# Optimization experiments

Hardware: AMD Instinct MI355X
Metric: run time of the kernel (lower is better)

Reference implementation:

```python
import jax, jax.numpy as jnp
import numpy as np

B, SIDES, L = 8192, 2, 64   # batch, (left,right) trees, leaves per tree (complete binary tree)
V, D, C, R = 10000, 128, 128, 7  # vocab, word_dim, cpr_dim, num_rels


def setup_inputs() -> dict:
    key = jax.random.key(0)
    ks = jax.random.split(key, 9)
    s = 0.05
    return {
        "tokens": jax.random.randint(ks[0], (B, SIDES, L), 0, V, dtype=jnp.int32),
        "voc_w": jax.random.normal(ks[1], (V, D), dtype=jnp.float32) * s,
        "voc_b": jax.random.normal(ks[2], (D,), dtype=jnp.float32) * s,
        "cps_w": jax.random.normal(ks[3], (D, 2 * D), dtype=jnp.float32) * s,
        "cps_b": jax.random.normal(ks[4], (D,), dtype=jnp.float32) * s,
        "cpr_w": jax.random.normal(ks[5], (C, 2 * D), dtype=jnp.float32) * s,
        "cpr_b": jax.random.normal(ks[6], (C,), dtype=jnp.float32) * s,
        "sm_w": jax.random.normal(ks[7], (R, C), dtype=jnp.float32) * s,
        "sm_b": jax.random.normal(ks[8], (R,), dtype=jnp.float32) * s,
    }


def reference(tokens, voc_w, voc_b, cps_w, cps_b, cpr_w, cpr_b, sm_w, sm_b):
    # Leaf composition: one-hot @ Linear(voc_size, word_dim) == embedding gather + bias
    h = voc_w[tokens] + voc_b  # [B, 2, L, D]
    # Level-by-level composition of complete binary trees: cat(left,right) -> cps -> tanh
    n = h.shape[2]
    while n > 1:
        h = h.reshape(h.shape[0], SIDES, n // 2, 2 * h.shape[-1])  # adjacent pairs -> concat
        h = jnp.tanh(jnp.einsum('bsnk,dk->bsnd', h, cps_w) + cps_b)
        n //= 2
    root = h.reshape(h.shape[0], -1)  # [B, 2*D]: cat(left_cps, right_cps)
    z = jax.nn.leaky_relu(root @ cpr_w.T + cpr_b)  # LeakyReLU default slope 0.01
    return jax.nn.softmax(z @ sm_w.T + sm_b, axis=-1)  # [B, R]
```

## Files before the change

kernel.cpp:

```cpp
#include <hip/hip_runtime.h>
#include <hip/hip_bf16.h>


typedef __attribute__((ext_vector_type(8))) short bf16x8;
typedef __attribute__((ext_vector_type(4))) float f32x4;

#define VOCN (10000 * 128)
#define CPSN (128 * 256)
#define CPRN (128 * 256)

__device__ __forceinline__ uint pk2(float a, float b) {
  union { __hip_bfloat162 h2; uint u; } cv;
  cv.h2 = __float22bfloat162_rn(make_float2(a, b));
  return cv.u;
}
__device__ __forceinline__ float2 up2(uint u) {
  union { uint u; __hip_bfloat162 h2; } cv; cv.u = u;
  return __bfloat1622float2(cv.h2);
}
__device__ __forceinline__ float fast_tanh(float x) {
  float e = __builtin_amdgcn_exp2f(x * 2.88539008f);
  return 1.0f - 2.0f * __builtin_amdgcn_rcpf(e + 1.0f);
}

__global__ void prep_kernel(const float* __restrict__ voc_w, const float* __restrict__ voc_b,
                            const float* __restrict__ cps_w, const float* __restrict__ cpr_w,
                            ushort* __restrict__ ws) {
  const int i4 = (blockIdx.x * 256 + threadIdx.x) * 4;
  if (i4 >= VOCN + CPSN + CPRN) return;
  float4 v;
  if (i4 < VOCN) {
    v = *(const float4*)(voc_w + i4);
    const float4 bb = *(const float4*)(voc_b + (i4 & 127));
    v.x += bb.x; v.y += bb.y; v.z += bb.z; v.w += bb.w;
  } else if (i4 < VOCN + CPSN) {
    v = *(const float4*)(cps_w + (i4 - VOCN));
  } else {
    v = *(const float4*)(cpr_w + (i4 - VOCN - CPSN));
  }
  uint2 w; w.x = pk2(v.x, v.y); w.y = pk2(v.z, v.w);
  *(uint2*)(ws + i4) = w;
}

#define MFMA16(Ax, Bx, Cx) __builtin_amdgcn_mfma_f32_16x16x32_bf16(Ax, Bx, Cx, 0, 0, 0)

template<int TOFF>
__device__ __forceinline__ void tile16(const char* hb, const bf16x8 (&A)[2][8],
                                       int RL, int RR, f32x4& aA, f32x4& aB) {
  bf16x8 bl[4], br[4];
#pragma unroll
  for (int q = 0; q < 4; ++q) {
    bl[q] = *(const bf16x8*)(hb + RL + TOFF + q * 4096);
    br[q] = *(const bf16x8*)(hb + RR + TOFF + q * 4096);
  }
#pragma unroll
  for (int q = 0; q < 4; ++q) {
    aA = MFMA16(A[0][q], bl[q], aA);
    aB = MFMA16(A[1][q], bl[q], aB);
  }
#pragma unroll
  for (int q = 0; q < 4; ++q) {
    aA = MFMA16(A[0][4 + q], br[q], aA);
    aB = MFMA16(A[1][4 + q], br[q], aB);
  }
}

template<int TOFF>
__device__ __forceinline__ void wtile(char* hb, int W, const f32x4& aA, const f32x4& aB) {
  uint2 w0, w1;
  w0.x = pk2(fast_tanh(aA[0]), fast_tanh(aA[1]));
  w0.y = pk2(fast_tanh(aA[2]), fast_tanh(aA[3]));
  w1.x = pk2(fast_tanh(aB[0]), fast_tanh(aB[1]));
  w1.y = pk2(fast_tanh(aB[2]), fast_tanh(aB[3]));
  *(uint2*)(hb + W + TOFF) = w0;
  *(uint2*)(hb + W + TOFF + 2048) = w1;
}

template<int PRE>
__global__ __launch_bounds__(256, 4)
void trnn_kernel(const int* __restrict__ tokens,
                 const float* __restrict__ voc_w, const float* __restrict__ voc_b,
                 const float* __restrict__ cps_w, const float* __restrict__ cps_b,
                 const float* __restrict__ cpr_w, const float* __restrict__ cpr_b,
                 const float* __restrict__ sm_w, const float* __restrict__ sm_b,
                 const ushort* __restrict__ wsb, float* __restrict__ out) {
  __shared__ ushort h[16384];
  const int tid = threadIdx.x;
  const int lane = tid & 63, wv = tid >> 6;
  const int l15 = lane & 15, lh = lane >> 4;
  const int b = blockIdx.x;
  char* hb = (char*)h;

  const ushort* voc_bf = wsb;
  const ushort* cps_bf = wsb + VOCN;
  const ushort* cpr_bf = wsb + VOCN + CPSN;

  const int lhb = lh * 1024;
  const int lb16 = l15 * 16;
  const int RLa = lhb + lb16;
  const int RLb = lhb + 256 + lb16;
  const int RRa = lhb + 512 + lb16;
  const int RRb = lhb + 768 + lb16;
  const int t3 = ((l15 >> 3) & 1) << 14;
  const int RL3 = t3 + lhb + (l15 & 7) * 16;
  const int RR3 = RL3 + 128;
  const int t4 = ((l15 >> 2) & 1) << 14;
  const int RL4 = t4 + lhb + (l15 & 3) * 16;
  const int RR4 = RL4 + 64;
  const int t5 = ((l15 >> 1) & 1) << 14;
  const int RL5 = t5 + lhb + (l15 & 1) * 16;
  const int RR5 = RL5 + 32;
  const int t6 = (l15 & 1) << 14;
  const int RL6 = t6 + lhb;
  const int RR6 = RL6 + 16;
  const int dpart = (((wv * 32 + lh * 4) >> 3) << 10) + ((lh & 1) << 3);
  const int Wa = ((l15 & 1) * 16 + (l15 >> 1)) * 16 + dpart;
  const int Wb = Wa + 128;
  const int W2 = ((l15 & 1) * 8 + (l15 >> 1)) * 16 + dpart;
  const int W3 = t3 + (((l15 & 1) * 4 + ((l15 & 7) >> 1)) * 16) + dpart;
  const int W4 = t4 + (((l15 & 1) * 2 + ((l15 & 3) >> 1)) * 16) + dpart;
  const int W5 = t5 + ((l15 & 1) * 16) + dpart;
  const int W6 = t6 + dpart;

  bf16x8 A[2][8];
  f32x4 bias[2];
#pragma unroll
  for (int mt = 0; mt < 2; ++mt) {
    const int d = wv * 32 + mt * 16 + l15;
#pragma unroll
    for (int kt = 0; kt < 8; ++kt) {
      const int k = kt * 32 + lh * 8;
      if constexpr (PRE) {
        A[mt][kt] = *(const bf16x8*)(cps_bf + d * 256 + k);
      } else {
        const float* p = cps_w + d * 256 + k;
        float4 lo = *(const float4*)p, hi = *(const float4*)(p + 4);
        union { bf16x8 v; uint4 u; } f;
        f.u.x = pk2(lo.x, lo.y); f.u.y = pk2(lo.z, lo.w);
        f.u.z = pk2(hi.x, hi.y); f.u.w = pk2(hi.z, hi.w);
        A[mt][kt] = f.v;
      }
    }
    const float4 bb = *(const float4*)(cps_b + wv * 32 + mt * 16 + lh * 4);
    bias[mt][0] = bb.x; bias[mt][1] = bb.y; bias[mt][2] = bb.z; bias[mt][3] = bb.w;
  }

  {
    const int tree = tid >> 7, lf = (tid >> 1) & 63, half = tid & 1;
    const int tok = tokens[b * 128 + tree * 64 + lf];
    const int p = (lf & 1) * 32 + (lf >> 1);
    char* tp = hb + tree * 16384 + half * 8192 + p * 16;
    if constexpr (PRE) {
      const ushort* vr = voc_bf + tok * 128 + half * 64;
#pragma unroll
      for (int j = 0; j < 8; ++j) {
        const int c = (j + p) & 7;
        *(uint4*)(tp + c * 1024) = *(const uint4*)(vr + c * 8);
      }
    } else {
      const float* vw = voc_w + tok * 128 + half * 64;
      const float* vb = voc_b + half * 64;
#pragma unroll
      for (int j = 0; j < 8; ++j) {
        const int c = (j + p) & 7;
        float4 v0 = *(const float4*)(vw + c * 8);
        float4 v1 = *(const float4*)(vw + c * 8 + 4);
        float4 q0 = *(const float4*)(vb + c * 8);
        float4 q1 = *(const float4*)(vb + c * 8 + 4);
        uint4 w;
        w.x = pk2(v0.x + q0.x, v0.y + q0.y);
        w.y = pk2(v0.z + q0.z, v0.w + q0.w);
        w.z = pk2(v1.x + q1.x, v1.y + q1.y);
        w.w = pk2(v1.z + q1.z, v1.w + q1.w);
        *(uint4*)(tp + c * 1024) = w;
      }
    }
  }
  __syncthreads();

  {
    f32x4 a0 = bias[0], b0 = bias[1], a1 = bias[0], b1 = bias[1];
    f32x4 a2 = bias[0], b2 = bias[1], a3 = bias[0], b3 = bias[1];
    tile16<0>(hb, A, RLa, RRa, a0, b0);
    tile16<0>(hb, A, RLb, RRb, a1, b1);
    tile16<16384>(hb, A, RLa, RRa, a2, b2);
    tile16<16384>(hb, A, RLb, RRb, a3, b3);
    __syncthreads();
    wtile<0>(hb, Wa, a0, b0);
    wtile<0>(hb, Wb, a1, b1);
    wtile<16384>(hb, Wa, a2, b2);
    wtile<16384>(hb, Wb, a3, b3);
    __syncthreads();
  }
  {
    f32x4 a0 = bias[0], b0 = bias[1], a1 = bias[0], b1 = bias[1];
    tile16<0>(hb, A, RLa, RLb, a0, b0);
    tile16<16384>(hb, A, RLa, RLb, a1, b1);
    __syncthreads();
    wtile<0>(hb, W2, a0, b0);
    wtile<16384>(hb, W2, a1, b1);
    __syncthreads();
  }
  {
    f32x4 a0 = bias[0], b0 = bias[1];
    tile16<0>(hb, A, RL3, RR3, a0, b0);
    __syncthreads();
    wtile<0>(hb, W3, a0, b0);
    __syncthreads();
  }
  {
    f32x4 a0 = bias[0], b0 = bias[1];
    tile16<0>(hb, A, RL4, RR4, a0, b0);
    __syncthreads();
    if (l15 < 8) wtile<0>(hb, W4, a0, b0);
    __syncthreads();
  }
  {
    f32x4 a0 = bias[0], b0 = bias[1];
    tile16<0>(hb, A, RL5, RR5, a0, b0);
    __syncthreads();
    if (l15 < 4) wtile<0>(hb, W5, a0, b0);
    __syncthreads();
  }
  {
    f32x4 a0 = bias[0], b0 = bias[1];
    tile16<0>(hb, A, RL6, RR6, a0, b0);
    __syncthreads();
    if (l15 < 2) wtile<0>(hb, W6, a0, b0);
    __syncthreads();
  }


  {
    const int half = tid >> 7, c = tid & 127;
    const char* rp = hb + half * 16384;
    float acc = 0.f;
#pragma unroll 4
    for (int ch = 0; ch < 16; ++ch) {
      uint4 u = *(const uint4*)(rp + ch * 1024);
      float2 e0 = up2(u.x), e1 = up2(u.y), e2 = up2(u.z), e3 = up2(u.w);
      if constexpr (PRE) {
        uint4 wq = *(const uint4*)(cpr_bf + c * 256 + half * 128 + ch * 8);
        float2 w0 = up2(wq.x), w1 = up2(wq.y), w2 = up2(wq.z), w3 = up2(wq.w);
        acc += e0.x * w0.x + e0.y * w0.y + e1.x * w1.x + e1.y * w1.y
             + e2.x * w2.x + e2.y * w2.y + e3.x * w3.x + e3.y * w3.y;
      } else {
        const float* wr = cpr_w + c * 256 + half * 128 + ch * 8;
        float4 w0 = *(const float4*)wr, w1 = *(const float4*)(wr + 4);
        acc += e0.x * w0.x + e0.y * w0.y + e1.x * w0.z + e1.y * w0.w
             + e2.x * w1.x + e2.y * w1.y + e3.x * w1.z + e3.y * w1.w;
      }
    }
    *(float*)(hb + ((tid >> 4) << 10) + 512 + ((tid & 15) << 2)) = acc;
  }
  __syncthreads();
  if (tid < 128) {
    const float p0 = *(const float*)(hb + ((tid >> 4) << 10) + 512 + ((tid & 15) << 2));
    const int j1 = tid + 128;
    const float p1 = *(const float*)(hb + ((j1 >> 4) << 10) + 512 + ((j1 & 15) << 2));
    float z = p0 + p1 + cpr_b[tid];
    z = z > 0.f ? z : 0.01f * z;
    *(float*)(hb + 16384 + ((tid >> 3) << 10) + 768 + ((tid & 7) << 2)) = z;
  }
  __syncthreads();

  if (wv == 0) {
    const int i0 = lane, i1 = 64 + lane;
    const float za = *(const float*)(hb + 16384 + ((i0 >> 3) << 10) + 768 + ((i0 & 7) << 2));
    const float zc = *(const float*)(hb + 16384 + ((i1 >> 3) << 10) + 768 + ((i1 & 7) << 2));
    float p[7];
#pragma unroll
    for (int j = 0; j < 7; ++j)
      p[j] = za * sm_w[j * 128 + lane] + zc * sm_w[j * 128 + 64 + lane];
#pragma unroll
    for (int j = 0; j < 7; ++j) {
      float v = p[j];
#pragma unroll
      for (int off = 32; off >= 1; off >>= 1) v += __shfl_xor(v, off, 64);
      p[j] = v + sm_b[j];
    }
    float mx = p[0];
#pragma unroll
    for (int j = 1; j < 7; ++j) mx = fmaxf(mx, p[j]);
    float e[7], s = 0.f;
#pragma unroll
    for (int j = 0; j < 7; ++j) { e[j] = __expf(p[j] - mx); s += e[j]; }
    const float inv = 1.f / s;
    if (lane == 0) {
#pragma unroll
      for (int j = 0; j < 7; ++j) out[b * 7 + j] = e[j] * inv;
    }
  }
}

extern "C" void kernel_launch(void* const* d_in, const int* in_sizes, int n_in,
                              void* d_out, int out_size, void* d_ws, size_t ws_size,
                              hipStream_t stream) {
  const int*   tokens = (const int*)  d_in[0];
  const float* voc_w  = (const float*)d_in[1];
  const float* voc_b  = (const float*)d_in[2];
  const float* cps_w  = (const float*)d_in[3];
  const float* cps_b  = (const float*)d_in[4];
  const float* cpr_w  = (const float*)d_in[5];
  const float* cpr_b  = (const float*)d_in[6];
  const float* sm_w   = (const float*)d_in[7];
  const float* sm_b   = (const float*)d_in[8];
  float* out = (float*)d_out;

  const int B = in_sizes[0] / 128;
  const size_t need = (size_t)(VOCN + CPSN + CPRN) * sizeof(ushort);

  if (ws_size >= need) {
    ushort* ws = (ushort*)d_ws;
    const int tot4 = (VOCN + CPSN + CPRN) / 4;
    prep_kernel<<<(tot4 + 255) / 256, 256, 0, stream>>>(voc_w, voc_b, cps_w, cpr_w, ws);
    trnn_kernel<1><<<B, 256, 0, stream>>>(tokens, voc_w, voc_b, cps_w, cps_b,
                                          cpr_w, cpr_b, sm_w, sm_b, ws, out);
  } else {
    trnn_kernel<0><<<B, 256, 0, stream>>>(tokens, voc_w, voc_b, cps_w, cps_b,
                                          cpr_w, cpr_b, sm_w, sm_b,
                                          (const ushort*)d_ws, out);
  }
}
```

Baseline: 162.3 us.

## Process two batch elements per block and prefetch next embeddings during the tail

Each block now handles two consecutive batch samples, so the per-block load of the composition weights into registers is paid once for two trees. The leaf embeddings for the second sample are fetched into registers before the projection and softmax stage of the first sample, then written to shared memory afterwards to hide gather latency. The leaky-ReLU outputs move to a separate small shared array so the next leaves can be stored safely. The costs are half as many blocks, extra registers for the prefetch buffer, and an unrotated store order for the second sample's leaves that may add shared-memory bank conflicts.

```diff
diff --git a/kernel.cpp b/kernel.cpp
--- a/kernel.cpp
+++ b/kernel.cpp
@@ -85,10 +85,11 @@
                  const float* __restrict__ sm_w, const float* __restrict__ sm_b,
                  const ushort* __restrict__ wsb, float* __restrict__ out) {
   __shared__ ushort h[16384];
+  __shared__ float z2[128];
   const int tid = threadIdx.x;
   const int lane = tid & 63, wv = tid >> 6;
   const int l15 = lane & 15, lh = lane >> 4;
-  const int b = blockIdx.x;
+  const int b0 = blockIdx.x * 2;
   char* hb = (char*)h;
 
   const ushort* voc_bf = wsb;
@@ -145,24 +146,24 @@
     bias[mt][0] = bb.x; bias[mt][1] = bb.y; bias[mt][2] = bb.z; bias[mt][3] = bb.w;
   }
 
+  const int tree_e = tid >> 7, lf_e = (tid >> 1) & 63, half_e = tid & 1;
+  const int p_e = (lf_e & 1) * 32 + (lf_e >> 1);
+  char* tp = hb + tree_e * 16384 + half_e * 8192 + p_e * 16;
   {
-    const int tree = tid >> 7, lf = (tid >> 1) & 63, half = tid & 1;
-    const int tok = tokens[b * 128 + tree * 64 + lf];
-    const int p = (lf & 1) * 32 + (lf >> 1);
-    char* tp = hb + tree * 16384 + half * 8192 + p * 16;
+    const int tok = tokens[b0 * 128 + tree_e * 64 + lf_e];
     if constexpr (PRE) {
-      const ushort* vr = voc_bf + tok * 128 + half * 64;
+      const ushort* vr = voc_bf + tok * 128 + half_e * 64;
 #pragma unroll
       for (int j = 0; j < 8; ++j) {
-        const int c = (j + p) & 7;
+        const int c = (j + p_e) & 7;
         *(uint4*)(tp + c * 1024) = *(const uint4*)(vr + c * 8);
       }
     } else {
-      const float* vw = voc_w + tok * 128 + half * 64;
-      const float* vb = voc_b + half * 64;
+      const float* vw = voc_w + tok * 128 + half_e * 64;
+      const float* vb = voc_b + half_e * 64;
 #pragma unroll
       for (int j = 0; j < 8; ++j) {
-        const int c = (j + p) & 7;
+        const int c = (j + p_e) & 7;
         float4 v0 = *(const float4*)(vw + c * 8);
         float4 v1 = *(const float4*)(vw + c * 8 + 4);
         float4 q0 = *(const float4*)(vb + c * 8);
@@ -178,117 +179,150 @@
   }
   __syncthreads();
 
-  {
-    f32x4 a0 = bias[0], b0 = bias[1], a1 = bias[0], b1 = bias[1];
-    f32x4 a2 = bias[0], b2 = bias[1], a3 = bias[0], b3 = bias[1];
-    tile16<0>(hb, A, RLa, RRa, a0, b0);
-    tile16<0>(hb, A, RLb, RRb, a1, b1);
-    tile16<16384>(hb, A, RLa, RRa, a2, b2);
-    tile16<16384>(hb, A, RLb, RRb, a3, b3);
+  for (int r = 0; r < 2; ++r) {
+    {
+      f32x4 a0 = bias[0], b0v = bias[1], a1 = bias[0], b1 = bias[1];
+      f32x4 a2 = bias[0], b2 = bias[1], a3 = bias[0], b3 = bias[1];
+      tile16<0>(hb, A, RLa, RRa, a0, b0v);
+      tile16<0>(hb, A, RLb, RRb, a1, b1);
+      tile16<16384>(hb, A, RLa, RRa, a2, b2);
+      tile16<16384>(hb, A, RLb, RRb, a3, b3);
+      __syncthreads();
+      wtile<0>(hb, Wa, a0, b0v);
+      wtile<0>(hb, Wb, a1, b1);
+      wtile<16384>(hb, Wa, a2, b2);
+      wtile<16384>(hb, Wb, a3, b3);
+      __syncthreads();
+    }
+    {
+      f32x4 a0 = bias[0], b0v = bias[1], a1 = bias[0], b1 = bias[1];
+      tile16<0>(hb, A, RLa, RLb, a0, b0v);
+      tile16<16384>(hb, A, RLa, RLb, a1, b1);
+      __syncthreads();
+      wtile<0>(hb, W2, a0, b0v);
+      wtile<16384>(hb, W2, a1, b1);
+      __syncthreads();
+    }
+    {
+      f32x4 a0 = bias[0], b0v = bias[1];
+      tile16<0>(hb, A, RL3, RR3, a0, b0v);
+      __syncthreads();
+      wtile<0>(hb, W3, a0, b0v);
+      __syncthreads();
+    }
+    {
+      f32x4 a0 = bias[0], b0v = bias[1];
+      tile16<0>(hb, A, RL4, RR4, a0, b0v);
+      __syncthreads();
+      if (l15 < 8) wtile<0>(hb, W4, a0, b0v);
+      __syncthreads();
+    }
+    {
+      f32x4 a0 = bias[0], b0v = bias[1];
+      tile16<0>(hb, A, RL5, RR5, a0, b0v);
+      __syncthreads();
+      if (l15 < 4) wtile<0>(hb, W5, a0, b0v);
+      __syncthreads();
+    }
+    {
+      f32x4 a0 = bias[0], b0v = bias[1];
+      tile16<0>(hb, A, RL6, RR6, a0, b0v);
+      __syncthreads();
+      if (l15 < 2) wtile<0>(hb, W6, a0, b0v);
+      __syncthreads();
+    }
+
+    uint4 pf[8];
+    if (PRE && r == 0) {
+      const int tok1 = tokens[(b0 + 1) * 128 + tree_e * 64 + lf_e];
+      const ushort* vr = voc_bf + tok1 * 128 + half_e * 64;
+#pragma unroll
+      for (int j = 0; j < 8; ++j) pf[j] = *(const uint4*)(vr + j * 8);
+    }
+
+    {
+      const int half = tid >> 7, c = tid & 127;
+      const char* rp = hb + half * 16384;
+      float acc = 0.f;
+#pragma unroll 4
+      for (int ch = 0; ch < 16; ++ch) {
+        uint4 u = *(const uint4*)(rp + ch * 1024);
+        float2 e0 = up2(u.x), e1 = up2(u.y), e2 = up2(u.z), e3 = up2(u.w);
+        if constexpr (PRE) {
+          uint4 wq = *(const uint4*)(cpr_bf + c * 256 + half * 128 + ch * 8);
+          float2 w0 = up2(wq.x), w1 = up2(wq.y), w2 = up2(wq.z), w3 = up2(wq.w);
+          acc += e0.x * w0.x + e0.y * w0.y + e1.x * w1.x + e1.y * w1.y
+               + e2.x * w2.x + e2.y * w2.y + e3.x * w3.x + e3.y * w3.y;
+        } else {
+          const float* wr = cpr_w + c * 256 + half * 128 + ch * 8;
+          float4 w0 = *(const float4*)wr, w1 = *(const float4*)(wr + 4);
+          acc += e0.x * w0.x + e0.y * w0.y + e1.x * w0.z + e1.y * w0.w
+               + e2.x * w1.x + e2.y * w1.y + e3.x * w1.z + e3.y * w1.w;
+        }
+      }
+      *(float*)(hb + ((tid >> 4) << 10) + 512 + ((tid & 15) << 2)) = acc;
+    }
     __syncthreads();
-    wtile<0>(hb, Wa, a0, b0);
-    wtile<0>(hb, Wb, a1, b1);
-    wtile<16384>(hb, Wa, a2, b2);
-    wtile<16384>(hb, Wb, a3, b3);
+    if (tid < 128) {
+      const float p0 = *(const float*)(hb + ((tid >> 4) << 10) + 512 + ((tid & 15) << 2));
+      const int j1 = tid + 128;
+      const float p1 = *(const float*)(hb + ((j1 >> 4) << 10) + 512 + ((j1 & 15) << 2));
+      float z = p0 + p1 + cpr_b[tid];
+      z2[tid] = z > 0.f ? z : 0.01f * z;
+    }
     __syncthreads();
-  }
-  {
-    f32x4 a0 = bias[0], b0 = bias[1], a1 = bias[0], b1 = bias[1];
-    tile16<0>(hb, A, RLa, RLb, a0, b0);
-    tile16<16384>(hb, A, RLa, RLb, a1, b1);
-    __syncthreads();
-    wtile<0>(hb, W2, a0, b0);
-    wtile<16384>(hb, W2, a1, b1);
-    __syncthreads();
-  }
-  {
-    f32x4 a0 = bias[0], b0 = bias[1];
-    tile16<0>(hb, A, RL3, RR3, a0, b0);
-    __syncthreads();
-    wtile<0>(hb, W3, a0, b0);
-    __syncthreads();
-  }
-  {
-    f32x4 a0 = bias[0], b0 = bias[1];
-    tile16<0>(hb, A, RL4, RR4, a0, b0);
-    __syncthreads();
-    if (l15 < 8) wtile<0>(hb, W4, a0, b0);
-    __syncthreads();
-  }
-  {
-    f32x4 a0 = bias[0], b0 = bias[1];
-    tile16<0>(hb, A, RL5, RR5, a0, b0);
-    __syncthreads();
-    if (l15 < 4) wtile<0>(hb, W5, a0, b0);
-    __syncthreads();
-  }
-  {
-    f32x4 a0 = bias[0], b0 = bias[1];
-    tile16<0>(hb, A, RL6, RR6, a0, b0);
-    __syncthreads();
-    if (l15 < 2) wtile<0>(hb, W6, a0, b0);
-    __syncthreads();
-  }
-
-
-  {
-    const int half = tid >> 7, c = tid & 127;
-    const char* rp = hb + half * 16384;
-    float acc = 0.f;
-#pragma unroll 4
-    for (int ch = 0; ch < 16; ++ch) {
-      uint4 u = *(const uint4*)(rp + ch * 1024);
-      float2 e0 = up2(u.x), e1 = up2(u.y), e2 = up2(u.z), e3 = up2(u.w);
+
+    if (wv == 0) {
+      const float za = z2[lane];
+      const float zc = z2[64 + lane];
+      float p[7];
+#pragma unroll
+      for (int j = 0; j < 7; ++j)
+        p[j] = za * sm_w[j * 128 + lane] + zc * sm_w[j * 128 + 64 + lane];
+#pragma unroll
+      for (int j = 0; j < 7; ++j) {
+        float v = p[j];
+#pragma unroll
+        for (int off = 32; off >= 1; off >>= 1) v += __shfl_xor(v, off, 64);
+        p[j] = v + sm_b[j];
+      }
+      float mx = p[0];
+#pragma unroll
+      for (int j = 1; j < 7; ++j) mx = fmaxf(mx, p[j]);
+      float e[7], s = 0.f;
+#pragma unroll
+      for (int j = 0; j < 7; ++j) { e[j] = __expf(p[j] - mx); s += e[j]; }
+      const float inv = 1.f / s;
+      if (lane == 0) {
+#pragma unroll
+        for (int j = 0; j < 7; ++j) out[(b0 + r) * 7 + j] = e[j] * inv;
+      }
+    }
+
+    if (r == 0) {
       if constexpr (PRE) {
-        uint4 wq = *(const uint4*)(cpr_bf + c * 256 + half * 128 + ch * 8);
-        float2 w0 = up2(wq.x), w1 = up2(wq.y), w2 = up2(wq.z), w3 = up2(wq.w);
-        acc += e0.x * w0.x + e0.y * w0.y + e1.x * w1.x + e1.y * w1.y
-             + e2.x * w2.x + e2.y * w2.y + e3.x * w3.x + e3.y * w3.y;
+#pragma unroll
+        for (int j = 0; j < 8; ++j)
+          *(uint4*)(tp + j * 1024) = pf[j];
       } else {
-        const float* wr = cpr_w + c * 256 + half * 128 + ch * 8;
-        float4 w0 = *(const float4*)wr, w1 = *(const float4*)(wr + 4);
-        acc += e0.x * w0.x + e0.y * w0.y + e1.x * w0.z + e1.y * w0.w
-             + e2.x * w1.x + e2.y * w1.y + e3.x * w1.z + e3.y * w1.w;
-      }
-    }
-    *(float*)(hb + ((tid >> 4) << 10) + 512 + ((tid & 15) << 2)) = acc;
-  }
-  __syncthreads();
-  if (tid < 128) {
-    const float p0 = *(const float*)(hb + ((tid >> 4) << 10) + 512 + ((tid & 15) << 2));
-    const int j1 = tid + 128;
-    const float p1 = *(const float*)(hb + ((j1 >> 4) << 10) + 512 + ((j1 & 15) << 2));
-    float z = p0 + p1 + cpr_b[tid];
-    z = z > 0.f ? z : 0.01f * z;
-    *(float*)(hb + 16384 + ((tid >> 3) << 10) + 768 + ((tid & 7) << 2)) = z;
-  }
-  __syncthreads();
-
-  if (wv == 0) {
-    const int i0 = lane, i1 = 64 + lane;
-    const float za = *(const float*)(hb + 16384 + ((i0 >> 3) << 10) + 768 + ((i0 & 7) << 2));
-    const float zc = *(const float*)(hb + 16384 + ((i1 >> 3) << 10) + 768 + ((i1 & 7) << 2));
-    float p[7];
-#pragma unroll
-    for (int j = 0; j < 7; ++j)
-      p[j] = za * sm_w[j * 128 + lane] + zc * sm_w[j * 128 + 64 + lane];
-#pragma unroll
-    for (int j = 0; j < 7; ++j) {
-      float v = p[j];
-#pragma unroll
-      for (int off = 32; off >= 1; off >>= 1) v += __shfl_xor(v, off, 64);
-      p[j] = v + sm_b[j];
-    }
-    float mx = p[0];
-#pragma unroll
-    for (int j = 1; j < 7; ++j) mx = fmaxf(mx, p[j]);
-    float e[7], s = 0.f;
-#pragma unroll
-    for (int j = 0; j < 7; ++j) { e[j] = __expf(p[j] - mx); s += e[j]; }
-    const float inv = 1.f / s;
-    if (lane == 0) {
-#pragma unroll
-      for (int j = 0; j < 7; ++j) out[b * 7 + j] = e[j] * inv;
+        const int tok = tokens[(b0 + 1) * 128 + tree_e * 64 + lf_e];
+        const float* vw = voc_w + tok * 128 + half_e * 64;
+        const float* vb = voc_b + half_e * 64;
+#pragma unroll
+        for (int j = 0; j < 8; ++j) {
+          float4 v0 = *(const float4*)(vw + j * 8);
+          float4 v1 = *(const float4*)(vw + j * 8 + 4);
+          float4 q0 = *(const float4*)(vb + j * 8);
+          float4 q1 = *(const float4*)(vb + j * 8 + 4);
+          uint4 w;
+          w.x = pk2(v0.x + q0.x, v0.y + q0.y);
+          w.y = pk2(v0.z + q0.z, v0.w + q0.w);
+          w.z = pk2(v1.x + q1.x, v1.y + q1.y);
+          w.w = pk2(v1.z + q1.z, v1.w + q1.w);
+          *(uint4*)(tp + j * 1024) = w;
+        }
+      }
+      __syncthreads();
     }
   }
 }
@@ -314,11 +348,11 @@
     ushort* ws = (ushort*)d_ws;
     const int tot4 = (VOCN + CPSN + CPRN) / 4;
     prep_kernel<<<(tot4 + 255) / 256, 256, 0, stream>>>(voc_w, voc_b, cps_w, cpr_w, ws);
-    trnn_kernel<1><<<B, 256, 0, stream>>>(tokens, voc_w, voc_b, cps_w, cps_b,
-                                          cpr_w, cpr_b, sm_w, sm_b, ws, out);
+    trnn_kernel<1><<<B / 2, 256, 0, stream>>>(tokens, voc_w, voc_b, cps_w, cps_b,
+                                              cpr_w, cpr_b, sm_w, sm_b, ws, out);
   } else {
-    trnn_kernel<0><<<B, 256, 0, stream>>>(tokens, voc_w, voc_b, cps_w, cps_b,
-                                          cpr_w, cpr_b, sm_w, sm_b,
-                                          (const ushort*)d_ws, out);
-  }
-}
+    trnn_kernel<0><<<B / 2, 256, 0, stream>>>(tokens, voc_w, voc_b, cps_w, cps_b,
+                                              cpr_w, cpr_b, sm_w, sm_b,
+                                              (const ushort*)d_ws, out);
+  }
+}
```

After: 247.2 us. 1.52x slower.
